# Kernel optimization log

Hardware: AMD Instinct MI355X
Metric: run time of the kernel (lower is better)

Reference implementation:

```python
import jax, jax.numpy as jnp
import numpy as np

B, T, HID = 2, 2048, 2048
H = 8
DK = 256   # head_qk_dim = hidden*expand_k/H
DV = 512   # head_v_dim  = hidden*expand_v/H
CH = 64    # chunk size
EPS = 1e-5
GLN = 16.0  # gate_logit_normalizer


def setup_inputs() -> dict:
    key = jax.random.key(0)
    ks = jax.random.split(key, 8)
    s = 0.02  # xavier-ish small init scale
    return {
        "x": jax.random.normal(ks[0], (B, T, HID), jnp.float32),
        "Wq": jax.random.normal(ks[1], (HID, H * DK), jnp.float32) * s,
        "Wk": jax.random.normal(ks[2], (HID, H * DK), jnp.float32) * s,
        "Wv": jax.random.normal(ks[3], (HID, H * DV), jnp.float32) * s,
        "Wg": jax.random.normal(ks[4], (HID, H * DV), jnp.float32) * s,
        "Wgk": jax.random.normal(ks[5], (HID, H), jnp.float32) * s,
        "bgk": jnp.zeros((H,), jnp.float32),
        "Wo": jax.random.normal(ks[6], (H * DV, HID), jnp.float32) * s,
        "norm_w": jnp.ones((DV,), jnp.float32),
    }


def chunk_simple_gla(q, k, v, gk):
    """q,k: [B,H,T,DK]; v: [B,H,T,DV]; gk: [B,H,T] (log-decay <= 0).
    Chunked recurrence: S_t = exp(gk_t) * S_{t-1} + k_t^T v_t; o_t = scale * q_t @ S_t."""
    scale = DK ** -0.5
    nc = T // CH
    # -> [NC, B, H, C, d] so lax.scan runs over chunks
    qc = q.reshape(B, H, nc, CH, DK).transpose(2, 0, 1, 3, 4)
    kc = k.reshape(B, H, nc, CH, DK).transpose(2, 0, 1, 3, 4)
    vc = v.reshape(B, H, nc, CH, DV).transpose(2, 0, 1, 3, 4)
    gc = jnp.cumsum(gk.reshape(B, H, nc, CH), axis=-1).transpose(2, 0, 1, 3)  # inclusive within-chunk cumsum

    idx = jnp.arange(CH)
    causal = idx[:, None] >= idx[None, :]

    def step(S, inp):
        qi, ki, vi, gi = inp          # gi: [B,H,C]
        gl = gi[..., -1:]             # total chunk decay [B,H,1]
        qs = qi * scale
        # inter-chunk: query decayed by cumulative gate times carried state
        o_inter = jnp.einsum('bhck,bhkv->bhcv', qs * jnp.exp(gi)[..., None], S)
        # intra-chunk causal attention with relative decay exp(G_i - G_j), i >= j
        diff = jnp.where(causal, gi[..., :, None] - gi[..., None, :], -jnp.inf)
        A = jnp.einsum('bhik,bhjk->bhij', qs, ki) * jnp.exp(diff)
        o = o_inter + jnp.einsum('bhij,bhjv->bhiv', A, vi)
        # state update: decay old state by full chunk, add keys decayed to chunk end
        S_new = jnp.exp(gl)[..., None] * S + jnp.einsum(
            'bhck,bhcv->bhkv', ki * jnp.exp(gl - gi)[..., None], vi)
        return S_new, o

    S0 = jnp.zeros((B, H, DK, DV), q.dtype)
    _, o = jax.lax.scan(step, S0, (qc, kc, vc, gc))  # o: [NC,B,H,C,DV]
    return o.transpose(1, 2, 0, 3, 4).reshape(B, H, T, DV)


def reference(x, Wq, Wk, Wv, Wg, Wgk, bgk, Wo, norm_w):
    q = (x @ Wq).reshape(B, T, H, DK).transpose(0, 2, 1, 3)  # [B,H,T,DK]
    k = (x @ Wk).reshape(B, T, H, DK).transpose(0, 2, 1, 3)
    v = (x @ Wv).reshape(B, T, H, DV).transpose(0, 2, 1, 3)
    gk = jax.nn.log_sigmoid(x @ Wgk + bgk) / GLN             # [B,T,H]
    gk = gk.transpose(0, 2, 1)                               # [B,H,T]
    o = chunk_simple_gla(q, k, v, gk)                        # [B,H,T,DV]
    o = o.transpose(0, 2, 1, 3)                              # [B,T,H,DV]
    # fused RMSNorm + swish gate (per head_v_dim)
    g = (x @ Wg).reshape(B, T, H, DV)
    on = o * jax.lax.rsqrt(jnp.mean(o * o, axis=-1, keepdims=True) + EPS) * norm_w
    o = on * (g * jax.nn.sigmoid(g))
    return o.reshape(B, T, H * DV) @ Wo
```

## Files before the change

### kernel.cpp

```cpp
#include <hip/hip_runtime.h>
#include <cstdint>
#include <cstddef>

#define NB 2
#define TSEQ 2048
#define HIDD 2048
#define NH 8
#define DKD 256
#define DVD 512
#define CHK 64
#define NCH 32
#define HDKD 2048
#define HDVD 4096

typedef __attribute__((ext_vector_type(8))) short s16x8;
typedef __attribute__((ext_vector_type(4))) float fx4;

__device__ __forceinline__ float bf2f(unsigned short u) {
  union { float f; uint32_t i; } x; x.i = ((uint32_t)u) << 16; return x.f;
}
__device__ __forceinline__ unsigned short f2bf(float f) {
  union { float f; uint32_t i; } x; x.f = f;
  uint32_t r = (x.i + 0x7fffu + ((x.i >> 16) & 1u)) >> 16;
  return (unsigned short)r;
}

__device__ __forceinline__ void gload16(const unsigned short* g, unsigned short* l) {
  __builtin_amdgcn_global_load_lds(
      (const __attribute__((address_space(1))) void*)g,
      (__attribute__((address_space(3))) void*)l, 16, 0, 0);
}

__global__ __launch_bounds__(256) void cast_f32_bf16(const float* __restrict__ in,
                                                     unsigned short* __restrict__ out, int n8) {
  int idx = blockIdx.x * 256 + threadIdx.x;
  if (idx >= n8) return;
  const float4* p = (const float4*)(in + (size_t)idx * 8);
  float4 a = p[0], b = p[1];
  unsigned short u[8];
  u[0]=f2bf(a.x); u[1]=f2bf(a.y); u[2]=f2bf(a.z); u[3]=f2bf(a.w);
  u[4]=f2bf(b.x); u[5]=f2bf(b.y); u[6]=f2bf(b.z); u[7]=f2bf(b.w);
  *(uint4*)(out + (size_t)idx * 8) = *(uint4*)u;
}

__global__ __launch_bounds__(256) void transpose_cast(const float* __restrict__ in,
                                                      unsigned short* __restrict__ out,
                                                      int R, int C) {
  __shared__ float tile[64][65];
  const int tid = threadIdx.x;
  const int c0 = blockIdx.x * 64, r0 = blockIdx.y * 64;
  #pragma unroll
  for (int it = 0; it < 4; ++it) {
    int idx = tid + it * 256;
    int row = idx >> 4, c4 = (idx & 15) * 4;
    float4 v = *(const float4*)(in + (size_t)(r0 + row) * C + c0 + c4);
    tile[row][c4 + 0] = v.x; tile[row][c4 + 1] = v.y;
    tile[row][c4 + 2] = v.z; tile[row][c4 + 3] = v.w;
  }
  __syncthreads();
  #pragma unroll
  for (int it = 0; it < 4; ++it) {
    int idx = tid + it * 256;
    int orow = idx >> 4, r4 = (idx & 15) * 4;
    ushort4 u;
    u.x = f2bf(tile[r4 + 0][orow]);
    u.y = f2bf(tile[r4 + 1][orow]);
    u.z = f2bf(tile[r4 + 2][orow]);
    u.w = f2bf(tile[r4 + 3][orow]);
    *(ushort4*)(out + (size_t)(c0 + orow) * R + r0 + r4) = u;
  }
}

__global__ __launch_bounds__(256) void bt_transpose(const unsigned short* __restrict__ in,
                                                    unsigned short* __restrict__ out,
                                                    int inW, int DF) {
  __shared__ unsigned short tile[64][65];
  const int tid = threadIdx.x;
  const int t0 = blockIdx.x * 64, c0 = blockIdx.y * 64;
  const int b = blockIdx.z >> 3, h = blockIdx.z & 7;
  #pragma unroll
  for (int it = 0; it < 2; ++it) {
    int idx = tid + it * 256;
    int tr = idx >> 3, tc0 = (idx & 7) * 8;
    uint4 v = *(const uint4*)(in + (size_t)(b * 2048 + t0 + tr) * inW + h * DF + c0 + tc0);
    const unsigned short* u = (const unsigned short*)&v;
    #pragma unroll
    for (int j = 0; j < 8; ++j) tile[tr][tc0 + j] = u[j];
  }
  __syncthreads();
  #pragma unroll
  for (int it = 0; it < 2; ++it) {
    int idx = tid + it * 256;
    int od = idx >> 3, ot0 = (idx & 7) * 8;
    unsigned short u[8];
    #pragma unroll
    for (int j = 0; j < 8; ++j) u[j] = tile[ot0 + j][od];
    *(uint4*)(out + ((size_t)blockIdx.z * DF + c0 + od) * 2048 + t0 + ot0) = *(uint4*)u;
  }
}

__global__ __launch_bounds__(256) void gk_proj(const float* __restrict__ x,
                                               const float* __restrict__ Wgk,
                                               const float* __restrict__ bgk,
                                               float* __restrict__ gk) {
  const int row = blockIdx.x, tid = threadIdx.x;
  const float* xr = x + (size_t)row * HIDD;
  float acc[8];
  #pragma unroll
  for (int h = 0; h < 8; ++h) acc[h] = 0.f;
  for (int i = tid; i < HIDD; i += 256) {
    float xv = xr[i];
    const float4* wr = (const float4*)(Wgk + (size_t)i * 8);
    float4 w0 = wr[0], w1 = wr[1];
    acc[0] += xv * w0.x; acc[1] += xv * w0.y; acc[2] += xv * w0.z; acc[3] += xv * w0.w;
    acc[4] += xv * w1.x; acc[5] += xv * w1.y; acc[6] += xv * w1.z; acc[7] += xv * w1.w;
  }
  #pragma unroll
  for (int off = 32; off; off >>= 1) {
    #pragma unroll
    for (int h = 0; h < 8; ++h) acc[h] += __shfl_xor(acc[h], off, 64);
  }
  __shared__ float red[4][8];
  if ((tid & 63) == 0) {
    #pragma unroll
    for (int h = 0; h < 8; ++h) red[tid >> 6][h] = acc[h];
  }
  __syncthreads();
  if (tid < 8) {
    float z = red[0][tid] + red[1][tid] + red[2][tid] + red[3][tid] + bgk[tid];
    float ls = fminf(z, 0.f) - log1pf(__expf(-fabsf(z)));
    gk[(size_t)row * 8 + tid] = ls * (1.0f / 16.0f);
  }
}

template<int OUT_BF16>
__global__ __launch_bounds__(256, 2) void gemm_bt(const unsigned short* __restrict__ A,
                                                  const unsigned short* __restrict__ BT,
                                                  void* __restrict__ C,
                                                  int M, int N, int K) {
  __shared__ unsigned short smem[16384];
  unsigned short* As = smem;
  unsigned short* Bs = smem + 8192;
  const int tid = threadIdx.x, l = tid & 63;
  const int l15 = l & 15, l4 = l >> 4;
  const int w = tid >> 6, wm = w >> 1, wn = w & 1;
  const int m0 = blockIdx.y * 128, n0 = blockIdx.x * 128;
  const int nk = K >> 6;

  fx4 zero = {0.f, 0.f, 0.f, 0.f};
  fx4 acc[4][4];
  #pragma unroll
  for (int mi = 0; mi < 4; ++mi)
    #pragma unroll
    for (int ni = 0; ni < 4; ++ni) acc[mi][ni] = zero;

  const int srow[4] = { (w*4+0)*8 + (l>>3), (w*4+1)*8 + (l>>3), (w*4+2)*8 + (l>>3), (w*4+3)*8 + (l>>3) };
  const int soct[4] = { (l&7) ^ (srow[0]&7), (l&7) ^ (srow[1]&7), (l&7) ^ (srow[2]&7), (l&7) ^ (srow[3]&7) };

  for (int kt = 0; kt < nk; ++kt) {
    #pragma unroll
    for (int i = 0; i < 4; ++i) {
      gload16(A  + (size_t)(m0 + srow[i]) * K + kt * 64 + soct[i] * 8, As + (w*4+i)*512);
      gload16(BT + (size_t)(n0 + srow[i]) * K + kt * 64 + soct[i] * 8, Bs + (w*4+i)*512);
    }
    __syncthreads();
    #pragma unroll
    for (int ks = 0; ks < 2; ++ks) {
      s16x8 af[4], bf[4];
      #pragma unroll
      for (int i = 0; i < 4; ++i) {
        int arow = wm * 64 + i * 16 + l15;
        af[i] = *(const s16x8*)(As + arow * 64 + (((ks*4 + l4) ^ (arow & 7)) << 3));
        int brow = wn * 64 + i * 16 + l15;
        bf[i] = *(const s16x8*)(Bs + brow * 64 + (((ks*4 + l4) ^ (brow & 7)) << 3));
      }
      #pragma unroll
      for (int mi = 0; mi < 4; ++mi)
        #pragma unroll
        for (int ni = 0; ni < 4; ++ni)
          acc[mi][ni] = __builtin_amdgcn_mfma_f32_16x16x32_bf16(af[mi], bf[ni], acc[mi][ni], 0, 0, 0);
    }
    __syncthreads();
  }

  if (OUT_BF16) {
    #pragma unroll
    for (int mi = 0; mi < 4; ++mi)
      #pragma unroll
      for (int r = 0; r < 4; ++r) {
        int row = wm * 64 + mi * 16 + l4 * 4 + r;
        #pragma unroll
        for (int ni = 0; ni < 4; ++ni) {
          int col = wn * 64 + ni * 16 + l15;
          smem[row * 128 + (((col >> 3) ^ (row & 7)) << 3) + (col & 7)] = f2bf(acc[mi][ni][r]);
        }
      }
    __syncthreads();
    #pragma unroll
    for (int it = 0; it < 8; ++it) {
      int idx = tid + it * 256;
      int row = idx >> 4, cl = idx & 15;
      uint4 vv = *(const uint4*)(smem + row * 128 + ((cl ^ (row & 7)) << 3));
      *(uint4*)((unsigned short*)C + (size_t)(m0 + row) * N + n0 + cl * 8) = vv;
    }
  } else {
    #pragma unroll
    for (int mi = 0; mi < 4; ++mi)
      #pragma unroll
      for (int r = 0; r < 4; ++r) {
        const size_t row = m0 + wm * 64 + mi * 16 + l4 * 4 + r;
        #pragma unroll
        for (int ni = 0; ni < 4; ++ni) {
          const int col = n0 + wn * 64 + ni * 16 + l15;
          ((float*)C)[row * N + col] = acc[mi][ni][r];
        }
      }
  }
}

__global__ __launch_bounds__(256, 1) void gla_kernel(const unsigned short* __restrict__ qb,
                                                     const unsigned short* __restrict__ kb,
                                                     const unsigned short* __restrict__ ktg,
                                                     const unsigned short* __restrict__ vtg,
                                                     const float* __restrict__ gkw,
                                                     unsigned short* __restrict__ oat) {
  const int blk = blockIdx.x;
  const int bh = blk & 15, dvb = blk >> 4;
  const int b = bh >> 3, h = bh & 7;
  const int dv0 = dvb * 64;
  const int tid = threadIdx.x, l = tid & 63, w = tid >> 6;
  const int l15 = l & 15, l4 = l >> 4;

  __shared__ __align__(16) unsigned short skbuf[16384];
  __shared__ __align__(16) unsigned short qs[16384];
  __shared__ __align__(16) unsigned short kst[16384];
  __shared__ __align__(16) unsigned short vTs[2][4096];
  __shared__ __align__(16) unsigned short Als[4096];
  __shared__ float gis[64], els[64], eis[64];

  fx4 zero = {0.f, 0.f, 0.f, 0.f};
  fx4 S[16];
  #pragma unroll
  for (int t = 0; t < 16; ++t) S[t] = zero;

  const unsigned short* qbase = qb + (size_t)b * TSEQ * HDKD + h * DKD;
  const unsigned short* kbase = kb + (size_t)b * TSEQ * HDKD + h * DKD;
  const unsigned short* ktg_bh = ktg + (size_t)(b * 8 + h) * DKD * TSEQ;
  const unsigned short* vtg_bh = vtg + ((size_t)(b * 8 + h) * DVD + dv0) * TSEQ;
  const float*  gbase = gkw + (size_t)b * TSEQ * NH + h;
  unsigned short* obase = oat + (size_t)b * TSEQ * HDVD + h * DVD + dv0;

  const int dvl = w * 16 + l15;

  auto stage_qk = [&](int t0) {
    #pragma unroll
    for (int i = 0; i < 8; ++i) {
      int s = (w * 8 + i) * 64 + l;
      int row = s >> 5, o = s & 31;
      int osw = o ^ (row & 7);
      gload16(qbase + (size_t)(t0 + row) * HDKD + (osw << 3), qs  + (w * 8 + i) * 512);
      gload16(kbase + (size_t)(t0 + row) * HDKD + (osw << 3), kst + (w * 8 + i) * 512);
    }
  };
  auto stage_v = [&](int t0, int buf) {
    #pragma unroll
    for (int i = 0; i < 2; ++i) {
      int s = (w * 2 + i) * 64 + l;
      int dv = s >> 3, os = s & 7;
      gload16(vtg_bh + (size_t)dv * TSEQ + t0 + ((os ^ (dv & 7)) << 3), vTs[buf] + (w * 2 + i) * 512);
    }
  };

  stage_qk(0);
  stage_v(0, 0);

  for (int c = 0; c < NCH; ++c) {
    const int t0 = c * CHK;

    if (tid < 64) {
      float xg = gbase[(size_t)(t0 + tid) * NH];
      #pragma unroll
      for (int off = 1; off < 64; off <<= 1) {
        float y = __shfl_up(xg, off, 64);
        if (l >= off) xg += y;
      }
      gis[tid] = xg;
      float gl = __shfl(xg, 63, 64);
      els[tid] = __expf(gl - xg);
      eis[tid] = 0.0625f * __expf(xg);
    }
    #pragma unroll
    for (int t = 0; t < 16; ++t) {
      const int dk0 = t * 16 + l4 * 4;
      ushort4 p;
      p.x = f2bf(S[t].x); p.y = f2bf(S[t].y); p.z = f2bf(S[t].z); p.w = f2bf(S[t].w);
      *(ushort4*)(skbuf + dvl * 256 + (((dk0 >> 3) ^ (dvl & 7)) << 3) + (dk0 & 7)) = p;
    }
    __syncthreads();

    s16x8 kf[8], stf[8];
    #pragma unroll
    for (int ks = 0; ks < 8; ++ks) {
      kf[ks]  = *(const s16x8*)(kst   + dvl * 256 + (((ks * 4 + l4) ^ (dvl & 7)) << 3));
      stf[ks] = *(const s16x8*)(skbuf + dvl * 256 + (((ks * 4 + l4) ^ (dvl & 7)) << 3));
    }
    fx4 o1[4], ar[4];
    #pragma unroll
    for (int ct = 0; ct < 4; ++ct) {
      o1[ct] = zero; ar[ct] = zero;
      const int qrow = ct * 16 + l15;
      #pragma unroll
      for (int ks = 0; ks < 8; ++ks) {
        s16x8 qf = *(const s16x8*)(qs + qrow * 256 + (((ks * 4 + l4) ^ (l15 & 7)) << 3));
        o1[ct] = __builtin_amdgcn_mfma_f32_16x16x32_bf16(qf, stf[ks], o1[ct], 0, 0, 0);
        ar[ct] = __builtin_amdgcn_mfma_f32_16x16x32_bf16(qf, kf[ks], ar[ct], 0, 0, 0);
      }
    }
    {
      const int j = dvl;
      const float gj = gis[j];
      #pragma unroll
      for (int ct = 0; ct < 4; ++ct) {
        #pragma unroll
        for (int r = 0; r < 4; ++r) {
          const int i = ct * 16 + l4 * 4 + r;
          float av = (i >= j) ? ar[ct][r] * 0.0625f * __expf(gis[i] - gj) : 0.f;
          Als[i * 64 + (((j >> 3) ^ (i & 7)) << 3) + (j & 7)] = f2bf(av);
          o1[ct][r] *= eis[i];
        }
      }
    }
    __syncthreads();

    #pragma unroll
    for (int i = 0; i < 8; ++i) {
      int c16 = (w * 8 + i) * 64 + l;
      int dk = c16 >> 3, os = c16 & 7;
      gload16(ktg_bh + (size_t)dk * TSEQ + t0 + ((os ^ (dk & 7)) << 3), skbuf + (w * 8 + i) * 512);
    }
    s16x8 vf[2], vf2[2];
    #pragma unroll
    for (int ks = 0; ks < 2; ++ks)
      vf[ks] = *(const s16x8*)(vTs[c & 1] + dvl * 64 + (((ks * 4 + l4) ^ (dvl & 7)) << 3));
    #pragma unroll
    for (int ks = 0; ks < 2; ++ks)
      #pragma unroll
      for (int j = 0; j < 8; ++j) {
        float e = els[ks * 32 + l4 * 8 + j];
        vf2[ks][j] = (short)f2bf(bf2f((unsigned short)vf[ks][j]) * e);
      }
    #pragma unroll
    for (int ct = 0; ct < 4; ++ct) {
      const int i = ct * 16 + l15;
      #pragma unroll
      for (int ks = 0; ks < 2; ++ks) {
        s16x8 af = *(const s16x8*)(Als + i * 64 + (((ks * 4 + l4) ^ (i & 7)) << 3));
        o1[ct] = __builtin_amdgcn_mfma_f32_16x16x32_bf16(af, vf[ks], o1[ct], 0, 0, 0);
      }
      #pragma unroll
      for (int r = 0; r < 4; ++r) {
        const int tt = t0 + ct * 16 + l4 * 4 + r;
        obase[(size_t)tt * HDVD + dvl] = f2bf(o1[ct][r]);
      }
    }
    __syncthreads();

    {
      const int cn = (c + 1 < NCH) ? c + 1 : c;
      stage_qk(cn * CHK);
      stage_v(cn * CHK, (c + 1) & 1);
    }
    {
      const float egl = __expf(gis[63]);
      #pragma unroll
      for (int t = 0; t < 16; ++t) {
        S[t].x *= egl; S[t].y *= egl; S[t].z *= egl; S[t].w *= egl;
        const int dk = t * 16 + l15;
        #pragma unroll
        for (int ks = 0; ks < 2; ++ks) {
          s16x8 ktf = *(const s16x8*)(skbuf + dk * 64 + (((ks * 4 + l4) ^ (dk & 7)) << 3));
          S[t] = __builtin_amdgcn_mfma_f32_16x16x32_bf16(ktf, vf2[ks], S[t], 0, 0, 0);
        }
      }
    }
    __syncthreads();
  }
}

__global__ __launch_bounds__(256) void norm_gate(unsigned short* __restrict__ o,
                                                 const unsigned short* __restrict__ g,
                                                 const float* __restrict__ nw) {
  const int seg = blockIdx.x * 4 + (threadIdx.x >> 6);
  const int l = threadIdx.x & 63;
  const size_t base = (size_t)seg * 512 + l * 8;
  uint4 ov = *(const uint4*)(o + base);
  const unsigned short* ou = (const unsigned short*)&ov;
  float f[8], ss = 0.f;
  #pragma unroll
  for (int j = 0; j < 8; ++j) { f[j] = bf2f(ou[j]); ss += f[j] * f[j]; }
  #pragma unroll
  for (int off = 32; off; off >>= 1) ss += __shfl_xor(ss, off, 64);
  const float rms = rsqrtf(ss * (1.0f / 512.0f) + 1e-5f);
  uint4 gv = *(const uint4*)(g + base);
  const unsigned short* gu = (const unsigned short*)&gv;
  const float4 w0 = *(const float4*)(nw + l * 8);
  const float4 w1 = *(const float4*)(nw + l * 8 + 4);
  float wv[8] = {w0.x, w0.y, w0.z, w0.w, w1.x, w1.y, w1.z, w1.w};
  unsigned short ru[8];
  #pragma unroll
  for (int j = 0; j < 8; ++j) {
    float gf = bf2f(gu[j]);
    float si = gf / (1.f + __expf(-gf));
    ru[j] = f2bf(f[j] * rms * wv[j] * si);
  }
  *(uint4*)(o + base) = *(uint4*)ru;
}

extern "C" void kernel_launch(void* const* d_in, const int* in_sizes, int n_in,
                              void* d_out, int out_size, void* d_ws, size_t ws_size,
                              hipStream_t stream) {
  (void)in_sizes; (void)n_in; (void)out_size; (void)ws_size;
  const float* x   = (const float*)d_in[0];
  const float* Wq  = (const float*)d_in[1];
  const float* Wk  = (const float*)d_in[2];
  const float* Wv  = (const float*)d_in[3];
  const float* Wg  = (const float*)d_in[4];
  const float* Wgk = (const float*)d_in[5];
  const float* bgk = (const float*)d_in[6];
  const float* Wo  = (const float*)d_in[7];
  const float* nw  = (const float*)d_in[8];

  char* ws = (char*)d_ws;
  const size_t MB = 1024 * 1024;
  unsigned short* xb  = (unsigned short*)(ws + 0);
  unsigned short* wqT = (unsigned short*)(ws + 16*MB);
  unsigned short* wkT = (unsigned short*)(ws + 24*MB);
  unsigned short* wvT = (unsigned short*)(ws + 32*MB);
  unsigned short* wgT = (unsigned short*)(ws + 48*MB);
  unsigned short* woT = (unsigned short*)(ws + 64*MB);
  unsigned short* qb  = (unsigned short*)(ws + 80*MB);
  unsigned short* kb  = (unsigned short*)(ws + 96*MB);
  unsigned short* vb  = (unsigned short*)(ws + 112*MB);
  unsigned short* gb  = (unsigned short*)(ws + 144*MB);
  float* gkb          = (float*)(ws + 176*MB);
  unsigned short* ktg = wqT;
  unsigned short* vtg = wvT;
  unsigned short* oat = vb;

  cast_f32_bf16<<<4096, 256, 0, stream>>>(x, xb, 4096 * 2048 / 8);
  transpose_cast<<<dim3(32, 32), 256, 0, stream>>>(Wq, wqT, 2048, 2048);
  transpose_cast<<<dim3(32, 32), 256, 0, stream>>>(Wk, wkT, 2048, 2048);
  transpose_cast<<<dim3(64, 32), 256, 0, stream>>>(Wv, wvT, 2048, 4096);
  transpose_cast<<<dim3(64, 32), 256, 0, stream>>>(Wg, wgT, 2048, 4096);
  transpose_cast<<<dim3(32, 64), 256, 0, stream>>>(Wo, woT, 4096, 2048);
  gk_proj<<<4096, 256, 0, stream>>>(x, Wgk, bgk, gkb);

  gemm_bt<1><<<dim3(16, 32), 256, 0, stream>>>(xb, wqT, qb, 4096, 2048, 2048);
  gemm_bt<1><<<dim3(16, 32), 256, 0, stream>>>(xb, wkT, kb, 4096, 2048, 2048);
  gemm_bt<1><<<dim3(32, 32), 256, 0, stream>>>(xb, wvT, vb, 4096, 4096, 2048);
  gemm_bt<1><<<dim3(32, 32), 256, 0, stream>>>(xb, wgT, gb, 4096, 4096, 2048);

  bt_transpose<<<dim3(32, 4, 16), 256, 0, stream>>>(kb, ktg, 2048, 256);
  bt_transpose<<<dim3(32, 8, 16), 256, 0, stream>>>(vb, vtg, 4096, 512);

  gla_kernel<<<128, 256, 0, stream>>>(qb, kb, ktg, vtg, gkb, oat);
  norm_gate<<<8192, 256, 0, stream>>>(oat, gb, nw);

  gemm_bt<0><<<dim3(16, 32), 256, 0, stream>>>(oat, woT, d_out, 4096, 2048, 4096);
}
```

Measured before the change: 726.9 us.

## Double-buffer GEMM LDS tiles and split GLA scan across more blocks and waves

The GEMM now double-buffers its A/B tiles in shared memory, issuing the loads for the next K-tile before computing on the current one, so one barrier per iteration overlaps load with MFMA. The GLA recurrence kernel is repartitioned: each block handles 32 value columns instead of 64, giving 256 blocks of 512 threads arranged as a 4x2 wave grid. Each wave now holds a quarter of the state rows and a 16-row slice of the chunk outputs. This raises parallelism for the sequential chunk scan, which previously used only 128 blocks, at the cost of recomputing the intra-chunk attention (QK^T) in twice as many blocks and doubling GEMM shared-memory usage, which may lower occupancy.

After: 666.9 us. 1.09x faster.

```diff
diff --git a/kernel.cpp b/kernel.cpp
--- a/kernel.cpp
+++ b/kernel.cpp
@@ -138,9 +138,7 @@
                                                   const unsigned short* __restrict__ BT,
                                                   void* __restrict__ C,
                                                   int M, int N, int K) {
-  __shared__ unsigned short smem[16384];
-  unsigned short* As = smem;
-  unsigned short* Bs = smem + 8192;
+  __shared__ unsigned short smem[2][16384];
   const int tid = threadIdx.x, l = tid & 63;
   const int l15 = l & 15, l4 = l >> 4;
   const int w = tid >> 6, wm = w >> 1, wn = w & 1;
@@ -157,13 +155,21 @@
   const int srow[4] = { (w*4+0)*8 + (l>>3), (w*4+1)*8 + (l>>3), (w*4+2)*8 + (l>>3), (w*4+3)*8 + (l>>3) };
   const int soct[4] = { (l&7) ^ (srow[0]&7), (l&7) ^ (srow[1]&7), (l&7) ^ (srow[2]&7), (l&7) ^ (srow[3]&7) };
 
+  auto stage = [&](int kt, int buf) {
+    #pragma unroll
+    for (int i = 0; i < 4; ++i) {
+      gload16(A  + (size_t)(m0 + srow[i]) * K + kt * 64 + soct[i] * 8, smem[buf] + (w*4+i)*512);
+      gload16(BT + (size_t)(n0 + srow[i]) * K + kt * 64 + soct[i] * 8, smem[buf] + 8192 + (w*4+i)*512);
+    }
+  };
+
+  stage(0, 0);
+  __syncthreads();
   for (int kt = 0; kt < nk; ++kt) {
-    #pragma unroll
-    for (int i = 0; i < 4; ++i) {
-      gload16(A  + (size_t)(m0 + srow[i]) * K + kt * 64 + soct[i] * 8, As + (w*4+i)*512);
-      gload16(BT + (size_t)(n0 + srow[i]) * K + kt * 64 + soct[i] * 8, Bs + (w*4+i)*512);
-    }
-    __syncthreads();
+    const int cur = kt & 1;
+    if (kt + 1 < nk) stage(kt + 1, cur ^ 1);
+    const unsigned short* As = smem[cur];
+    const unsigned short* Bs = smem[cur] + 8192;
     #pragma unroll
     for (int ks = 0; ks < 2; ++ks) {
       s16x8 af[4], bf[4];
@@ -184,6 +190,7 @@
   }
 
   if (OUT_BF16) {
+    unsigned short* cs = smem[0];
     #pragma unroll
     for (int mi = 0; mi < 4; ++mi)
       #pragma unroll
@@ -192,7 +199,7 @@
         #pragma unroll
         for (int ni = 0; ni < 4; ++ni) {
           int col = wn * 64 + ni * 16 + l15;
-          smem[row * 128 + (((col >> 3) ^ (row & 7)) << 3) + (col & 7)] = f2bf(acc[mi][ni][r]);
+          cs[row * 128 + (((col >> 3) ^ (row & 7)) << 3) + (col & 7)] = f2bf(acc[mi][ni][r]);
         }
       }
     __syncthreads();
@@ -200,7 +207,7 @@
     for (int it = 0; it < 8; ++it) {
       int idx = tid + it * 256;
       int row = idx >> 4, cl = idx & 15;
-      uint4 vv = *(const uint4*)(smem + row * 128 + ((cl ^ (row & 7)) << 3));
+      uint4 vv = *(const uint4*)(cs + row * 128 + ((cl ^ (row & 7)) << 3));
       *(uint4*)((unsigned short*)C + (size_t)(m0 + row) * N + n0 + cl * 8) = vv;
     }
   } else {
@@ -218,7 +225,7 @@
   }
 }
 
-__global__ __launch_bounds__(256, 1) void gla_kernel(const unsigned short* __restrict__ qb,
+__global__ __launch_bounds__(512, 1) void gla_kernel(const unsigned short* __restrict__ qb,
                                                      const unsigned short* __restrict__ kb,
                                                      const unsigned short* __restrict__ ktg,
                                                      const unsigned short* __restrict__ vtg,
@@ -227,21 +234,22 @@
   const int blk = blockIdx.x;
   const int bh = blk & 15, dvb = blk >> 4;
   const int b = bh >> 3, h = bh & 7;
-  const int dv0 = dvb * 64;
+  const int dv0 = dvb * 32;
   const int tid = threadIdx.x, l = tid & 63, w = tid >> 6;
+  const int wr = w >> 1, wc = w & 1;
   const int l15 = l & 15, l4 = l >> 4;
 
   __shared__ __align__(16) unsigned short skbuf[16384];
   __shared__ __align__(16) unsigned short qs[16384];
   __shared__ __align__(16) unsigned short kst[16384];
-  __shared__ __align__(16) unsigned short vTs[2][4096];
+  __shared__ __align__(16) unsigned short vTs[2][2048];
   __shared__ __align__(16) unsigned short Als[4096];
   __shared__ float gis[64], els[64], eis[64];
 
   fx4 zero = {0.f, 0.f, 0.f, 0.f};
-  fx4 S[16];
-  #pragma unroll
-  for (int t = 0; t < 16; ++t) S[t] = zero;
+  fx4 S[4];
+  #pragma unroll
+  for (int t = 0; t < 4; ++t) S[t] = zero;
 
   const unsigned short* qbase = qb + (size_t)b * TSEQ * HDKD + h * DKD;
   const unsigned short* kbase = kb + (size_t)b * TSEQ * HDKD + h * DKD;
@@ -250,24 +258,24 @@
   const float*  gbase = gkw + (size_t)b * TSEQ * NH + h;
   unsigned short* obase = oat + (size_t)b * TSEQ * HDVD + h * DVD + dv0;
 
-  const int dvl = w * 16 + l15;
+  const int dvl = wc * 16 + l15;
+  const int irow = wr * 16 + l15;
 
   auto stage_qk = [&](int t0) {
     #pragma unroll
-    for (int i = 0; i < 8; ++i) {
-      int s = (w * 8 + i) * 64 + l;
+    for (int i = 0; i < 4; ++i) {
+      int s = (w * 4 + i) * 64 + l;
       int row = s >> 5, o = s & 31;
       int osw = o ^ (row & 7);
-      gload16(qbase + (size_t)(t0 + row) * HDKD + (osw << 3), qs  + (w * 8 + i) * 512);
-      gload16(kbase + (size_t)(t0 + row) * HDKD + (osw << 3), kst + (w * 8 + i) * 512);
+      gload16(qbase + (size_t)(t0 + row) * HDKD + (osw << 3), qs  + (w * 4 + i) * 512);
+      gload16(kbase + (size_t)(t0 + row) * HDKD + (osw << 3), kst + (w * 4 + i) * 512);
     }
   };
   auto stage_v = [&](int t0, int buf) {
-    #pragma unroll
-    for (int i = 0; i < 2; ++i) {
-      int s = (w * 2 + i) * 64 + l;
+    if (w < 4) {
+      int s = w * 64 + l;
       int dv = s >> 3, os = s & 7;
-      gload16(vtg_bh + (size_t)dv * TSEQ + t0 + ((os ^ (dv & 7)) << 3), vTs[buf] + (w * 2 + i) * 512);
+      gload16(vtg_bh + (size_t)dv * TSEQ + t0 + ((os ^ (dv & 7)) << 3), vTs[buf] + w * 512);
     }
   };
 
@@ -290,53 +298,47 @@
       eis[tid] = 0.0625f * __expf(xg);
     }
     #pragma unroll
-    for (int t = 0; t < 16; ++t) {
-      const int dk0 = t * 16 + l4 * 4;
+    for (int t = 0; t < 4; ++t) {
+      const int dk0 = wr * 64 + t * 16 + l4 * 4;
       ushort4 p;
       p.x = f2bf(S[t].x); p.y = f2bf(S[t].y); p.z = f2bf(S[t].z); p.w = f2bf(S[t].w);
       *(ushort4*)(skbuf + dvl * 256 + (((dk0 >> 3) ^ (dvl & 7)) << 3) + (dk0 & 7)) = p;
     }
     __syncthreads();
 
-    s16x8 kf[8], stf[8];
+    fx4 o1 = zero, ar[2] = {zero, zero};
     #pragma unroll
     for (int ks = 0; ks < 8; ++ks) {
-      kf[ks]  = *(const s16x8*)(kst   + dvl * 256 + (((ks * 4 + l4) ^ (dvl & 7)) << 3));
-      stf[ks] = *(const s16x8*)(skbuf + dvl * 256 + (((ks * 4 + l4) ^ (dvl & 7)) << 3));
-    }
-    fx4 o1[4], ar[4];
-    #pragma unroll
-    for (int ct = 0; ct < 4; ++ct) {
-      o1[ct] = zero; ar[ct] = zero;
-      const int qrow = ct * 16 + l15;
-      #pragma unroll
-      for (int ks = 0; ks < 8; ++ks) {
-        s16x8 qf = *(const s16x8*)(qs + qrow * 256 + (((ks * 4 + l4) ^ (l15 & 7)) << 3));
-        o1[ct] = __builtin_amdgcn_mfma_f32_16x16x32_bf16(qf, stf[ks], o1[ct], 0, 0, 0);
-        ar[ct] = __builtin_amdgcn_mfma_f32_16x16x32_bf16(qf, kf[ks], ar[ct], 0, 0, 0);
-      }
-    }
-    {
-      const int j = dvl;
+      s16x8 qf = *(const s16x8*)(qs + irow * 256 + (((ks * 4 + l4) ^ (irow & 7)) << 3));
+      s16x8 stf = *(const s16x8*)(skbuf + dvl * 256 + (((ks * 4 + l4) ^ (dvl & 7)) << 3));
+      o1 = __builtin_amdgcn_mfma_f32_16x16x32_bf16(qf, stf, o1, 0, 0, 0);
+      #pragma unroll
+      for (int jt = 0; jt < 2; ++jt) {
+        const int krow = wc * 32 + jt * 16 + l15;
+        s16x8 kf = *(const s16x8*)(kst + krow * 256 + (((ks * 4 + l4) ^ (krow & 7)) << 3));
+        ar[jt] = __builtin_amdgcn_mfma_f32_16x16x32_bf16(qf, kf, ar[jt], 0, 0, 0);
+      }
+    }
+    #pragma unroll
+    for (int jt = 0; jt < 2; ++jt) {
+      const int j = wc * 32 + jt * 16 + l15;
       const float gj = gis[j];
       #pragma unroll
-      for (int ct = 0; ct < 4; ++ct) {
-        #pragma unroll
-        for (int r = 0; r < 4; ++r) {
-          const int i = ct * 16 + l4 * 4 + r;
-          float av = (i >= j) ? ar[ct][r] * 0.0625f * __expf(gis[i] - gj) : 0.f;
-          Als[i * 64 + (((j >> 3) ^ (i & 7)) << 3) + (j & 7)] = f2bf(av);
-          o1[ct][r] *= eis[i];
-        }
-      }
-    }
-    __syncthreads();
-
-    #pragma unroll
-    for (int i = 0; i < 8; ++i) {
-      int c16 = (w * 8 + i) * 64 + l;
-      int dk = c16 >> 3, os = c16 & 7;
-      gload16(ktg_bh + (size_t)dk * TSEQ + t0 + ((os ^ (dk & 7)) << 3), skbuf + (w * 8 + i) * 512);
+      for (int r = 0; r < 4; ++r) {
+        const int i = wr * 16 + l4 * 4 + r;
+        float av = (i >= j) ? ar[jt][r] * 0.0625f * __expf(gis[i] - gj) : 0.f;
+        Als[i * 64 + (((j >> 3) ^ (i & 7)) << 3) + (j & 7)] = f2bf(av);
+      }
+    }
+    #pragma unroll
+    for (int r = 0; r < 4; ++r) o1[r] *= eis[wr * 16 + l4 * 4 + r];
+    __syncthreads();
+
+    #pragma unroll
+    for (int i = 0; i < 4; ++i) {
+      int s = (w * 4 + i) * 64 + l;
+      int dk = s >> 3, os = s & 7;
+      gload16(ktg_bh + (size_t)dk * TSEQ + t0 + ((os ^ (dk & 7)) << 3), skbuf + (w * 4 + i) * 512);
     }
     s16x8 vf[2], vf2[2];
     #pragma unroll
@@ -350,18 +352,14 @@
         vf2[ks][j] = (short)f2bf(bf2f((unsigned short)vf[ks][j]) * e);
       }
     #pragma unroll
-    for (int ct = 0; ct < 4; ++ct) {
-      const int i = ct * 16 + l15;
-      #pragma unroll
-      for (int ks = 0; ks < 2; ++ks) {
-        s16x8 af = *(const s16x8*)(Als + i * 64 + (((ks * 4 + l4) ^ (i & 7)) << 3));
-        o1[ct] = __builtin_amdgcn_mfma_f32_16x16x32_bf16(af, vf[ks], o1[ct], 0, 0, 0);
-      }
-      #pragma unroll
-      for (int r = 0; r < 4; ++r) {
-        const int tt = t0 + ct * 16 + l4 * 4 + r;
-        obase[(size_t)tt * HDVD + dvl] = f2bf(o1[ct][r]);
-      }
+    for (int ks = 0; ks < 2; ++ks) {
+      s16x8 af = *(const s16x8*)(Als + irow * 64 + (((ks * 4 + l4) ^ (irow & 7)) << 3));
+      o1 = __builtin_amdgcn_mfma_f32_16x16x32_bf16(af, vf[ks], o1, 0, 0, 0);
+    }
+    #pragma unroll
+    for (int r = 0; r < 4; ++r) {
+      const int tt = t0 + wr * 16 + l4 * 4 + r;
+      obase[(size_t)tt * HDVD + dvl] = f2bf(o1[r]);
     }
     __syncthreads();
 
@@ -373,9 +371,9 @@
     {
       const float egl = __expf(gis[63]);
       #pragma unroll
-      for (int t = 0; t < 16; ++t) {
+      for (int t = 0; t < 4; ++t) {
         S[t].x *= egl; S[t].y *= egl; S[t].z *= egl; S[t].w *= egl;
-        const int dk = t * 16 + l15;
+        const int dk = wr * 64 + t * 16 + l15;
         #pragma unroll
         for (int ks = 0; ks < 2; ++ks) {
           s16x8 ktf = *(const s16x8*)(skbuf + dk * 64 + (((ks * 4 + l4) ^ (dk & 7)) << 3));
@@ -463,7 +461,7 @@
   bt_transpose<<<dim3(32, 4, 16), 256, 0, stream>>>(kb, ktg, 2048, 256);
   bt_transpose<<<dim3(32, 8, 16), 256, 0, stream>>>(vb, vtg, 4096, 512);
 
-  gla_kernel<<<128, 256, 0, stream>>>(qb, kb, ktg, vtg, gkb, oat);
+  gla_kernel<<<256, 512, 0, stream>>>(qb, kb, ktg, vtg, gkb, oat);
   norm_gate<<<8192, 256, 0, stream>>>(oat, gb, nw);
 
   gemm_bt<0><<<dim3(16, 32), 256, 0, stream>>>(oat, woT, d_out, 4096, 2048, 4096);
```
